# Kernel tuning notes

Hardware: AMD Instinct MI355X
Metric: run time of the kernel (lower is better)

The kernel has to match this reference:

```python
import jax, jax.numpy as jnp
import numpy as np
from jax import lax

D_MODEL = 512
D_STATE = 64
D_CONV = 4
EXPAND = 2
HEADDIM = 64
D_INNER = EXPAND * D_MODEL          # 1024
NHEADS = D_INNER // HEADDIM         # 16
CONV_DIM = D_INNER + 2 * D_STATE    # 1152 (x, B, C go through depthwise conv)
D_PROJ = 2 * D_INNER + 2 * D_STATE + NHEADS  # 2192
EPS = 1e-5


def silu(x):
    return x * jax.nn.sigmoid(x)


def layernorm(x, w, b):
    mu = jnp.mean(x, axis=-1, keepdims=True)
    var = jnp.mean((x - mu) ** 2, axis=-1, keepdims=True)
    return (x - mu) * lax.rsqrt(var + EPS) * w + b


def mamba2(x, in_w, conv_w, conv_b, dt_bias, A_log, D_h, mnorm_w, out_w):
    """Faithful Mamba2 forward (sequential selective-scan form of SSD).
    x: [B, L, D_MODEL]"""
    Bsz, L, _ = x.shape
    zxbcdt = x @ in_w  # [B, L, D_PROJ]
    z = zxbcdt[..., :D_INNER]
    xBC = zxbcdt[..., D_INNER:D_INNER + CONV_DIM]
    dt = zxbcdt[..., -NHEADS:]

    # causal depthwise conv1d over sequence, then SiLU
    xBC_pad = jnp.pad(xBC, ((0, 0), (D_CONV - 1, 0), (0, 0)))
    xBC = lax.conv_general_dilated(
        xBC_pad, conv_w, window_strides=(1,), padding='VALID',
        dimension_numbers=('NWC', 'WIO', 'NWC'), feature_group_count=CONV_DIM)
    xBC = silu(xBC + conv_b)

    xh = xBC[..., :D_INNER].reshape(Bsz, L, NHEADS, HEADDIM)      # [B,L,H,P]
    Bc = xBC[..., D_INNER:D_INNER + D_STATE]                      # [B,L,N]
    Cc = xBC[..., D_INNER + D_STATE:]                             # [B,L,N]

    dt = jax.nn.softplus(dt + dt_bias)          # [B,L,H]
    dA = jnp.exp(dt * (-jnp.exp(A_log)))        # [B,L,H]
    dtx = dt[..., None] * xh                    # [B,L,H,P]

    def step(h, ins):
        dA_t, dtx_t, B_t, C_t = ins  # [B,H], [B,H,P], [B,N], [B,N]
        h = h * dA_t[:, :, None, None] + dtx_t[..., None] * B_t[:, None, None, :]
        y = jnp.einsum('bhpn,bn->bhp', h, C_t)
        return h, y

    h0 = jnp.zeros((Bsz, NHEADS, HEADDIM, D_STATE), x.dtype)
    xs = (jnp.moveaxis(dA, 1, 0), jnp.moveaxis(dtx, 1, 0),
          jnp.moveaxis(Bc, 1, 0), jnp.moveaxis(Cc, 1, 0))
    _, ys = lax.scan(step, h0, xs)              # [L,B,H,P]
    y = jnp.moveaxis(ys, 0, 1) + D_h[None, None, :, None] * xh
    y = y.reshape(Bsz, L, D_INNER)

    # gated RMSNorm: rmsnorm(y * silu(z)) * weight
    g = y * silu(z)
    g = g * lax.rsqrt(jnp.mean(g * g, axis=-1, keepdims=True) + EPS) * mnorm_w
    return g @ out_w  # [B, L, D_MODEL]


def setup_inputs() -> dict:
    key = jax.random.key(0)
    ks = jax.random.split(key, 16)
    B, L = 2, 4096
    s = 0.02
    inp = {
        'x': jax.random.normal(ks[0], (B, L, D_MODEL), jnp.float32),
        'norm_in_w': jnp.ones((D_MODEL,), jnp.float32),
        'norm_in_b': jnp.zeros((D_MODEL,), jnp.float32),
        'norm_out_w': jnp.ones((D_MODEL,), jnp.float32),
        'norm_out_b': jnp.zeros((D_MODEL,), jnp.float32),
        'in_w': jax.random.normal(ks[1], (D_MODEL, D_PROJ), jnp.float32) * s,
        'conv_w': jax.random.normal(ks[2], (D_CONV, 1, CONV_DIM), jnp.float32) * 0.1,
        'conv_b': jnp.zeros((CONV_DIM,), jnp.float32),
        'dt_bias': jnp.log(jnp.expm1(jax.random.uniform(ks[3], (NHEADS,), jnp.float32, 0.001, 0.1))),
        'A_log': jnp.log(jnp.arange(1, NHEADS + 1, dtype=jnp.float32)),
        'D_h': jnp.ones((NHEADS,), jnp.float32),
        'mnorm_w': jnp.ones((D_INNER,), jnp.float32),
        'out_w': jax.random.normal(ks[4], (D_INNER, D_MODEL), jnp.float32) * s,
        'ff_w1': jax.random.normal(ks[5], (D_MODEL, 4 * D_MODEL), jnp.float32) * s,
        'ff_b1': jnp.zeros((4 * D_MODEL,), jnp.float32),
        'ff_w2': jax.random.normal(ks[6], (4 * D_MODEL, D_MODEL), jnp.float32) * s,
        'ff_b2': jnp.zeros((D_MODEL,), jnp.float32),
    }
    return inp


def reference(x, norm_in_w, norm_in_b, norm_out_w, norm_out_b, in_w, conv_w,
              conv_b, dt_bias, A_log, D_h, mnorm_w, out_w, ff_w1, ff_b1,
              ff_w2, ff_b2):
    xn = layernorm(x, norm_in_w, norm_in_b)
    fwd = mamba2(xn, in_w, conv_w, conv_b, dt_bias, A_log, D_h, mnorm_w, out_w)
    bwd = mamba2(jnp.flip(xn, axis=1), in_w, conv_w, conv_b, dt_bias, A_log,
                 D_h, mnorm_w, out_w)
    m = layernorm(fwd + jnp.flip(bwd, axis=1), norm_out_w, norm_out_b)
    ff = jax.nn.gelu(m @ ff_w1 + ff_b1, approximate=False) @ ff_w2 + ff_b2
    return ff + x
```

## Files before the change

### kernel.cpp

```cpp
#include <hip/hip_runtime.h>
#include <hip/hip_bf16.h>

#define LSEQ 4096
#define BSZ 2
#define DMODEL 512
#define DINNER 1024
#define DSTATE 64
#define NHEADS 16
#define CONVDIM 1152
#define DPROJ 2192
#define NPAD 2304
#define NTOK (BSZ*LSEQ)
#define NCH 64

typedef __attribute__((ext_vector_type(8))) short short8;
typedef __attribute__((ext_vector_type(4))) float f32x4;

__device__ inline unsigned short f2b(float v){
  unsigned int u = __builtin_bit_cast(unsigned int, v);
  unsigned int r = (u + 0x7FFFu + ((u >> 16) & 1u)) >> 16;
  return (unsigned short)r;
}
__device__ inline float b2f(unsigned short u){
  unsigned int x = ((unsigned int)u) << 16;
  return __builtin_bit_cast(float, x);
}
__device__ inline uint4 pack8(const float* v){
  uint4 pk;
  pk.x = (unsigned)f2b(v[0]) | ((unsigned)f2b(v[1])<<16);
  pk.y = (unsigned)f2b(v[2]) | ((unsigned)f2b(v[3])<<16);
  pk.z = (unsigned)f2b(v[4]) | ((unsigned)f2b(v[5])<<16);
  pk.w = (unsigned)f2b(v[6]) | ((unsigned)f2b(v[7])<<16);
  return pk;
}
__device__ inline float gelu_f(float x){
  float x2 = x*x;
  float u = x*(0.7978845608f + 0.0356774081f*x2);
  float au = fabsf(u);
  float z = __expf(-2.f*au);
  float t = (1.f - z)/(1.f + z);
  t = (u >= 0.f) ? t : -t;
  return 0.5f*x*(1.f + t);
}

#define GLL16(gp, lp) __builtin_amdgcn_global_load_lds( \
    (const __attribute__((address_space(1))) unsigned int*)(gp), \
    (__attribute__((address_space(3))) unsigned int*)(lp), 16, 0, 0)

__global__ __launch_bounds__(256) void wconv_t(const float* __restrict__ src,
    unsigned short* __restrict__ dst, int K, int Nsrc, int Npad){
  __shared__ float t[32][33];
  int n0 = blockIdx.x*32, k0 = blockIdx.y*32;
  int tx = threadIdx.x & 31, ty = threadIdx.x >> 5;
  for (int i=0;i<4;i++){
    int k = k0 + ty + i*8; int n = n0 + tx;
    t[ty + i*8][tx] = (n < Nsrc) ? src[(size_t)k*Nsrc + n] : 0.f;
  }
  __syncthreads();
  for (int i=0;i<4;i++){
    int n = n0 + ty + i*8; int k = k0 + tx;
    if (n < Npad) dst[(size_t)n*K + k] = f2b(t[tx][ty + i*8]);
  }
}

__global__ __launch_bounds__(256) void layernorm_k(const float* __restrict__ in,
    const float* __restrict__ w, const float* __restrict__ bb, unsigned short* __restrict__ out){
  int row = blockIdx.x; int tid = threadIdx.x;
  const float* r = in + (size_t)row*DMODEL;
  float v0 = r[tid], v1 = r[tid+256];
  float s = v0+v1, sq = v0*v0+v1*v1;
  for (int m=32;m>=1;m>>=1){ s += __shfl_xor(s,m); sq += __shfl_xor(sq,m); }
  __shared__ float ws_[4], wq_[4];
  int wave = tid>>6, lane = tid&63;
  if (lane==0){ ws_[wave]=s; wq_[wave]=sq; }
  __syncthreads();
  s = ws_[0]+ws_[1]+ws_[2]+ws_[3]; sq = wq_[0]+wq_[1]+wq_[2]+wq_[3];
  float mu = s * (1.f/DMODEL);
  float var = sq * (1.f/DMODEL) - mu*mu;
  float rs = rsqrtf(var + 1e-5f);
  out[(size_t)row*DMODEL + tid]     = f2b((v0-mu)*rs*w[tid] + bb[tid]);
  out[(size_t)row*DMODEL + tid+256] = f2b((v1-mu)*rs*w[tid+256] + bb[tid+256]);
}

__global__ __launch_bounds__(256) void layernorm2_k(const float* __restrict__ in0,
    const float* __restrict__ in1,
    const float* __restrict__ w, const float* __restrict__ bb, unsigned short* __restrict__ out){
  int row = blockIdx.x; int tid = threadIdx.x;
  const float* r0 = in0 + (size_t)row*DMODEL;
  const float* r1 = in1 + (size_t)row*DMODEL;
  float v0 = r0[tid] + r1[tid], v1 = r0[tid+256] + r1[tid+256];
  float s = v0+v1, sq = v0*v0+v1*v1;
  for (int m=32;m>=1;m>>=1){ s += __shfl_xor(s,m); sq += __shfl_xor(sq,m); }
  __shared__ float ws_[4], wq_[4];
  int wave = tid>>6, lane = tid&63;
  if (lane==0){ ws_[wave]=s; wq_[wave]=sq; }
  __syncthreads();
  s = ws_[0]+ws_[1]+ws_[2]+ws_[3]; sq = wq_[0]+wq_[1]+wq_[2]+wq_[3];
  float mu = s * (1.f/DMODEL);
  float var = sq * (1.f/DMODEL) - mu*mu;
  float rs = rsqrtf(var + 1e-5f);
  out[(size_t)row*DMODEL + tid]     = f2b((v0-mu)*rs*w[tid] + bb[tid]);
  out[(size_t)row*DMODEL + tid+256] = f2b((v1-mu)*rs*w[tid+256] + bb[tid+256]);
}

__global__ __launch_bounds__(256) void reduce4_k(const float* __restrict__ pa,
    const float* __restrict__ pb, const float* __restrict__ bias,
    const float* __restrict__ resid, float* __restrict__ out){
  const size_t MN4 = (size_t)NTOK*DMODEL/4;
  for (size_t i = (size_t)blockIdx.x*256 + threadIdx.x; i < MN4; i += (size_t)gridDim.x*256){
    float4 a0 = ((const float4*)pa)[i];
    float4 a1 = ((const float4*)pa)[i + MN4];
    float4 b0 = ((const float4*)pb)[i];
    float4 b1 = ((const float4*)pb)[i + MN4];
    float4 rv = ((const float4*)resid)[i];
    int col = (int)((i*4) & (DMODEL-1));
    const float4 bs = *(const float4*)(bias + col);
    float4 o;
    o.x = a0.x + a1.x + b0.x + b1.x + bs.x + rv.x;
    o.y = a0.y + a1.y + b0.y + b1.y + bs.y + rv.y;
    o.z = a0.z + a1.z + b0.z + b1.z + bs.z + rv.z;
    o.w = a0.w + a1.w + b0.w + b1.w + bs.w + rv.w;
    ((float4*)out)[i] = o;
  }
}

__global__ __launch_bounds__(512, 2) void gemm256_k(const unsigned short* __restrict__ A,
    const unsigned short* __restrict__ Bt, void* __restrict__ outp, void* __restrict__ outp_hi,
    int M, int N, int K, int klen, int epi, const float* __restrict__ bias){
  __shared__ __align__(16) unsigned short As[32768];
  __shared__ __align__(16) unsigned short Bs[32768];
  const int tid = threadIdx.x;
  const int lane = tid & 63, wave = tid >> 6;
  const int wr = wave >> 2, wc = wave & 3;
  const int l15 = lane & 15, q = lane >> 4;
  int nbx = gridDim.x;
  int bid = blockIdx.y * nbx + blockIdx.x;
  int cpx = (nbx * gridDim.y) >> 3;
  int swz = (bid & 7) * cpx + (bid >> 3);
  int bn = swz % nbx, bm = swz / nbx;
  const int kstart = blockIdx.z * klen;
  const int NT = klen >> 6;
  const int j0 = tid, j1 = tid + 512;
  const int rr0 = j0 >> 2, rr1 = j1 >> 2;
  const int sc0 = (j0 & 3) ^ ((rr0 >> 1) & 3);
  const int sc1 = (j1 & 3) ^ ((rr1 >> 1) & 3);
  const unsigned short* a0 = A  + (size_t)(bm*256 + rr0)*K + kstart + sc0*8;
  const unsigned short* a1 = A  + (size_t)(bm*256 + rr1)*K + kstart + sc1*8;
  const unsigned short* b0 = Bt + (size_t)(bn*256 + rr0)*K + kstart + sc0*8;
  const unsigned short* b1 = Bt + (size_t)(bn*256 + rr1)*K + kstart + sc1*8;
  unsigned short* lA0 = As + j0*8;
  unsigned short* lA1 = As + j1*8;
  unsigned short* lB0 = Bs + j0*8;
  unsigned short* lB1 = Bs + j1*8;
#define STGA(t,kh) { const int go=(t)*64+(kh)*32, lo=((t)&1)*16384+(kh)*8192; \
  GLL16(a0+go, lA0+lo); GLL16(a1+go, lA1+lo); }
#define STGB(t,kh) { const int go=(t)*64+(kh)*32, lo=((t)&1)*16384+(kh)*8192; \
  GLL16(b0+go, lB0+lo); GLL16(b1+go, lB1+lo); }
  f32x4 acc[8][4];
  #pragma unroll
  for (int i=0;i<8;i++)
    #pragma unroll
    for (int j=0;j<4;j++) acc[i][j] = (f32x4){0.f,0.f,0.f,0.f};
  STGA(0,0); STGB(0,0); STGA(0,1); STGB(0,1);
  STGA(1,0); STGB(1,0);
  asm volatile("s_waitcnt vmcnt(4)" ::: "memory");
  __builtin_amdgcn_s_barrier();
  const int cOfs = (q ^ ((l15 >> 1) & 3)) * 8;
  const int arow = wr*128 + l15;
  const int brow = wc*64  + l15;
  for (int t = 0; t < NT; ++t){
    const unsigned short* Ab = As + (t & 1)*16384;
    const unsigned short* Bb = Bs + (t & 1)*16384;
    short8 af[4], bf4[4];
    #pragma unroll
    for (int mi=0;mi<4;mi++) af[mi]  = *(const short8*)(Ab + (arow + mi*16)*32 + cOfs);
    #pragma unroll
    for (int nt=0;nt<4;nt++) bf4[nt] = *(const short8*)(Bb + (brow + nt*16)*32 + cOfs);
    if (t+1 < NT) STGA(t+1,1);
    __builtin_amdgcn_s_barrier();
    asm volatile("s_waitcnt lgkmcnt(0)" ::: "memory");
    __builtin_amdgcn_sched_barrier(0);
    __builtin_amdgcn_s_setprio(1);
    #pragma unroll
    for (int mi=0;mi<4;mi++)
      #pragma unroll
      for (int nt=0;nt<4;nt++)
        acc[mi][nt] = __builtin_amdgcn_mfma_f32_16x16x32_bf16(af[mi], bf4[nt], acc[mi][nt], 0,0,0);
    __builtin_amdgcn_s_setprio(0);
    __builtin_amdgcn_s_barrier();
    #pragma unroll
    for (int mi=0;mi<4;mi++) af[mi] = *(const short8*)(Ab + (arow + (4+mi)*16)*32 + cOfs);
    if (t+1 < NT) STGB(t+1,1);
    __builtin_amdgcn_s_barrier();
    asm volatile("s_waitcnt lgkmcnt(0)" ::: "memory");
    __builtin_amdgcn_sched_barrier(0);
    __builtin_amdgcn_s_setprio(1);
    #pragma unroll
    for (int mi=0;mi<4;mi++)
      #pragma unroll
      for (int nt=0;nt<4;nt++)
        acc[4+mi][nt] = __builtin_amdgcn_mfma_f32_16x16x32_bf16(af[mi], bf4[nt], acc[4+mi][nt], 0,0,0);
    __builtin_amdgcn_s_setprio(0);
    __builtin_amdgcn_s_barrier();
    #pragma unroll
    for (int mi=0;mi<4;mi++) af[mi]  = *(const short8*)(Ab + 8192 + (arow + mi*16)*32 + cOfs);
    #pragma unroll
    for (int nt=0;nt<4;nt++) bf4[nt] = *(const short8*)(Bb + 8192 + (brow + nt*16)*32 + cOfs);
    if (t+2 < NT) STGA(t+2,0);
    __builtin_amdgcn_s_barrier();
    asm volatile("s_waitcnt lgkmcnt(0)" ::: "memory");
    __builtin_amdgcn_sched_barrier(0);
    __builtin_amdgcn_s_setprio(1);
    #pragma unroll
    for (int mi=0;mi<4;mi++)
      #pragma unroll
      for (int nt=0;nt<4;nt++)
        acc[mi][nt] = __builtin_amdgcn_mfma_f32_16x16x32_bf16(af[mi], bf4[nt], acc[mi][nt], 0,0,0);
    __builtin_amdgcn_s_setprio(0);
    __builtin_amdgcn_s_barrier();
    #pragma unroll
    for (int mi=0;mi<4;mi++) af[mi] = *(const short8*)(Ab + 8192 + (arow + (4+mi)*16)*32 + cOfs);
    if (t+2 < NT) STGB(t+2,0);
    __builtin_amdgcn_s_barrier();
    asm volatile("s_waitcnt lgkmcnt(0)" ::: "memory");
    __builtin_amdgcn_sched_barrier(0);
    __builtin_amdgcn_s_setprio(1);
    #pragma unroll
    for (int mi=0;mi<4;mi++)
      #pragma unroll
      for (int nt=0;nt<4;nt++)
        acc[4+mi][nt] = __builtin_amdgcn_mfma_f32_16x16x32_bf16(af[mi], bf4[nt], acc[4+mi][nt], 0,0,0);
    __builtin_amdgcn_s_setprio(0);
    if (t+2 < NT)      { asm volatile("s_waitcnt vmcnt(4)" ::: "memory"); }
    else if (t+1 < NT) { asm volatile("s_waitcnt vmcnt(0)" ::: "memory"); }
    __builtin_amdgcn_s_barrier();
  }
#undef STGA
#undef STGB
  float* cb = (float*)As + wave*1040;
  const int rbase = q*4;
  const int gr0t = bm*256 + wr*128;
  const int gc0 = bn*256 + wc*64;
  #pragma unroll
  for (int mt=0; mt<8; mt++){
    #pragma unroll
    for (int nt=0;nt<4;nt++)
      #pragma unroll
      for (int r=0;r<4;r++)
        cb[(rbase+r)*65 + nt*16 + l15] = acc[mt][nt][r];
    int gr0 = gr0t + mt*16;
    if (epi == 0){
      float* po = (float*)((blockIdx.z < 2) ? outp : outp_hi)
                + (size_t)(blockIdx.z & 1) * ((size_t)M * N);
      int r4 = lane >> 4, c0f = (lane & 15)*4;
      #pragma unroll
      for (int h=0; h<4; h++){
        int row = h*4 + r4;
        float4 v;
        v.x = cb[row*65 + c0f + 0];
        v.y = cb[row*65 + c0f + 1];
        v.z = cb[row*65 + c0f + 2];
        v.w = cb[row*65 + c0f + 3];
        *(float4*)(po + (size_t)(gr0+row)*N + gc0 + c0f) = v;
      }
    } else {
      int r8 = lane >> 3, c0 = (lane & 7)*8;
      #pragma unroll
      for (int h=0; h<2; h++){
        int row = h*8 + r8;
        float v[8];
        #pragma unroll
        for (int u=0;u<8;u++) v[u] = cb[row*65 + c0 + u];
        if (epi == 1){
          #pragma unroll
          for (int u=0;u<8;u++) v[u] = gelu_f(v[u] + bias[gc0 + c0 + u]);
        }
        *(uint4*)((unsigned short*)outp + (size_t)(gr0+row)*N + gc0 + c0) = pack8(v);
      }
    }
  }
}

__global__ __launch_bounds__(256) void dt_k(const unsigned short* __restrict__ zx,
    const float* __restrict__ dt_bias, const float* __restrict__ A_log,
    float* __restrict__ dAb, float* __restrict__ dtb){
  int b = blockIdx.y;
  int t = blockIdx.x*16 + (threadIdx.x>>4);
  int h = threadIdx.x & 15;
  float raw = b2f(zx[((size_t)b*LSEQ + t)*NPAD + (DINNER+CONVDIM) + h]) + dt_bias[h];
  float dt = (raw > 20.f) ? raw : log1pf(expf(raw));
  float dA = expf(-expf(A_log[h]) * dt);
  size_t f = ((size_t)b*LSEQ + t)*NHEADS + h;
  size_t r = ((size_t)(BSZ+b)*LSEQ + (LSEQ-1-t))*NHEADS + h;
  dAb[f] = dA; dtb[f] = dt;
  dAb[r] = dA; dtb[r] = dt;
}

__global__ __launch_bounds__(256) void conv_x_k(const unsigned short* __restrict__ zx,
    const float* __restrict__ conv_w, const float* __restrict__ conv_b,
    const float* __restrict__ dtb, unsigned short* __restrict__ dtxb,
    unsigned short* __restrict__ zcomp){
  int b = blockIdx.y;
  int t0blk = blockIdx.x * 32;
  int tid = threadIdx.x;
  int half = tid >> 7, cg = tid & 127;
  int c0 = cg * 8;
  int head = c0 >> 6;
  float wk[4][8], bias8[8];
  #pragma unroll
  for (int k=0;k<4;k++)
    #pragma unroll
    for (int j=0;j<8;j++) wk[k][j] = conv_w[k*CONVDIM + c0 + j];
  #pragma unroll
  for (int j=0;j<8;j++) bias8[j] = conv_b[c0 + j];
  __shared__ float sdtf[32][16], sdtb[32][16];
  for (int r = tid; r < 512; r += 256){
    int i = r >> 4, h = r & 15;
    sdtf[i][h] = dtb[((size_t)b*LSEQ + t0blk + i)*NHEADS + h];
    sdtb[i][h] = dtb[((size_t)(BSZ+b)*LSEQ + (LSEQ-1-(t0blk+i)))*NHEADS + h];
  }
  __syncthreads();
  int t0 = t0blk + half*16;
  float w0[8],w1[8],w2[8],w3[8];
  #pragma unroll
  for (int j=0;j<8;j++){ w1[j]=0.f; w2[j]=0.f; w3[j]=0.f; }
  for (int it=0; it<22; ++it){
    int t = t0 - 3 + it;
    #pragma unroll
    for (int j=0;j<8;j++){ w0[j]=w1[j]; w1[j]=w2[j]; w2[j]=w3[j]; }
    if (t >= 0 && t < LSEQ){
      uint4 xv = *(const uint4*)(zx + ((size_t)b*LSEQ + t)*NPAD + DINNER + c0);
      const unsigned short* xs = (const unsigned short*)&xv;
      #pragma unroll
      for (int j=0;j<8;j++) w3[j] = b2f(xs[j]);
      if (t >= t0 && t < t0+16){
        uint4 zv = *(const uint4*)(zx + ((size_t)b*LSEQ + t)*NPAD + c0);
        *(uint4*)(zcomp + ((size_t)b*LSEQ + t)*DINNER + c0) = zv;
      }
    } else {
      #pragma unroll
      for (int j=0;j<8;j++) w3[j] = 0.f;
    }
    if (t >= t0 && t < t0+16){
      float dtf = sdtf[t - t0blk][head];
      float v[8];
      #pragma unroll
      for (int j=0;j<8;j++){
        float a = bias8[j] + wk[0][j]*w0[j] + wk[1][j]*w1[j] + wk[2][j]*w2[j] + wk[3][j]*w3[j];
        v[j] = (a / (1.f + expf(-a))) * dtf;
      }
      *(uint4*)(dtxb + ((size_t)b*LSEQ + t)*DINNER + c0) = pack8(v);
    }
    int tau = t - 3;
    if (tau >= t0 && tau < t0+16){
      float dtv = sdtb[tau - t0blk][head];
      float v[8];
      #pragma unroll
      for (int j=0;j<8;j++){
        float a = bias8[j] + wk[0][j]*w3[j] + wk[1][j]*w2[j] + wk[2][j]*w1[j] + wk[3][j]*w0[j];
        v[j] = (a / (1.f + expf(-a))) * dtv;
      }
      *(uint4*)(dtxb + ((size_t)(BSZ+b)*LSEQ + (LSEQ-1-tau))*DINNER + c0) = pack8(v);
    }
  }
}

__global__ __launch_bounds__(256) void conv_bc_k(const unsigned short* __restrict__ zx,
    const float* __restrict__ conv_w, const float* __restrict__ conv_b,
    unsigned short* __restrict__ Bb, unsigned short* __restrict__ Cb){
  int b = blockIdx.y;
  int t0blk = blockIdx.x * 64;
  int tid = threadIdx.x;
  int slot = tid >> 4, cg = tid & 15;
  int c0 = cg*8;
  int ccol = DINNER + 1024 + c0;
  int cw = 1024 + c0;
  float wk[4][8], bias8[8];
  #pragma unroll
  for (int k=0;k<4;k++)
    #pragma unroll
    for (int j=0;j<8;j++) wk[k][j] = conv_w[k*CONVDIM + cw + j];
  #pragma unroll
  for (int j=0;j<8;j++) bias8[j] = conv_b[cw + j];
  int t0 = t0blk + slot*4;
  float w0[8],w1[8],w2[8],w3[8];
  #pragma unroll
  for (int j=0;j<8;j++){ w1[j]=0.f; w2[j]=0.f; w3[j]=0.f; }
  for (int it=0; it<10; ++it){
    int t = t0 - 3 + it;
    #pragma unroll
    for (int j=0;j<8;j++){ w0[j]=w1[j]; w1[j]=w2[j]; w2[j]=w3[j]; }
    if (t >= 0 && t < LSEQ){
      uint4 xv = *(const uint4*)(zx + ((size_t)b*LSEQ + t)*NPAD + ccol);
      const unsigned short* xs = (const unsigned short*)&xv;
      #pragma unroll
      for (int j=0;j<8;j++) w3[j] = b2f(xs[j]);
    } else {
      #pragma unroll
      for (int j=0;j<8;j++) w3[j] = 0.f;
    }
    if (t >= t0 && t < t0+4){
      float v[8];
      #pragma unroll
      for (int j=0;j<8;j++){
        float a = bias8[j] + wk[0][j]*w0[j] + wk[1][j]*w1[j] + wk[2][j]*w2[j] + wk[3][j]*w3[j];
        v[j] = a / (1.f + expf(-a));
      }
      size_t tok = (size_t)b*LSEQ + t;
      if (c0 < 64) *(uint4*)(Bb + tok*DSTATE + c0)      = pack8(v);
      else         *(uint4*)(Cb + tok*DSTATE + (c0-64)) = pack8(v);
    }
    int tau = t - 3;
    if (tau >= t0 && tau < t0+4){
      float v[8];
      #pragma unroll
      for (int j=0;j<8;j++){
        float a = bias8[j] + wk[0][j]*w3[j] + wk[1][j]*w2[j] + wk[2][j]*w1[j] + wk[3][j]*w0[j];
        v[j] = a / (1.f + expf(-a));
      }
      size_t tok = (size_t)(BSZ+b)*LSEQ + (LSEQ-1-tau);
      if (c0 < 64) *(uint4*)(Bb + tok*DSTATE + c0)      = pack8(v);
      else         *(uint4*)(Cb + tok*DSTATE + (c0-64)) = pack8(v);
    }
  }
}

__device__ inline void gemm64(const unsigned short* Ab, const unsigned short* Bb_,
                              int l15, int q, f32x4 acc[4][4]){
  #pragma unroll
  for (int ks=0; ks<2; ks++){
    short8 af[4], bf4[4];
    #pragma unroll
    for (int mt=0;mt<4;mt++) af[mt]  = *(const short8*)(Ab  + (mt*16+l15)*72 + ks*32 + q*8);
    #pragma unroll
    for (int nt=0;nt<4;nt++) bf4[nt] = *(const short8*)(Bb_ + (nt*16+l15)*72 + ks*32 + q*8);
    #pragma unroll
    for (int mt=0;mt<4;mt++)
      #pragma unroll
      for (int nt=0;nt<4;nt++)
        acc[mt][nt] = __builtin_amdgcn_mfma_f32_16x16x32_bf16(af[mt], bf4[nt], acc[mt][nt], 0,0,0);
  }
}

__global__ __launch_bounds__(64) void ssd1_k(const float* __restrict__ dAb,
    const unsigned short* __restrict__ dtxb, const unsigned short* __restrict__ Bb,
    const unsigned short* __restrict__ Cb,
    unsigned short* __restrict__ y0, unsigned short* __restrict__ y1,
    unsigned short* __restrict__ hbuf, float* __restrict__ Pch, float* __restrict__ ebuf){
  int ch = blockIdx.x, h = blockIdx.y, z = blockIdx.z;
  int d = z >> 1, b = z & 1;
  int lane = threadIdx.x;
  int l15 = lane & 15, q = lane >> 4;
  int tr = lane >> 3, cb8 = (lane & 7)*8;
  size_t tokb = (size_t)z*LSEQ + (size_t)ch*64;
  size_t zhc = ((size_t)z*NHEADS + h)*NCH + ch;
  __shared__ __align__(16) unsigned short S1[64*72];
  __shared__ __align__(16) unsigned short S2[64*72];
  __shared__ __align__(16) unsigned short S3[64*72];
  __shared__ float Lb[64];
  float L = fmaxf(logf(dAb[(tokb + lane)*NHEADS + h]), -60.f);
  #pragma unroll
  for (int off=1; off<64; off<<=1){
    float v = __shfl_up(L, off);
    if (lane >= off) L += v;
  }
  Lb[lane] = L;
  float e = expf(L);
  ebuf[zhc*64 + lane] = e;
  if (lane == 63) Pch[zhc] = e;
  for (int i=0;i<8;i++){
    int t = i*8 + tr;
    *(uint4*)&S1[t*72 + cb8] = *(const uint4*)(Cb + (tokb+t)*DSTATE + cb8);
    *(uint4*)&S2[t*72 + cb8] = *(const uint4*)(Bb + (tokb+t)*DSTATE + cb8);
    uint4 xv = *(const uint4*)(dtxb + (tokb+t)*DINNER + (size_t)h*64 + cb8);
    const unsigned short* xs = (const unsigned short*)&xv;
    #pragma unroll
    for (int j=0;j<8;j++) S3[(cb8+j)*72 + t] = xs[j];
  }
  f32x4 sa[4][4];
  for (int i=0;i<4;i++) for (int j=0;j<4;j++) sa[i][j] = (f32x4){0.f,0.f,0.f,0.f};
  gemm64(S1, S2, l15, q, sa);
  float Lsv[4];
  #pragma unroll
  for (int nt=0;nt<4;nt++) Lsv[nt] = Lb[nt*16 + l15];
  #pragma unroll
  for (int mt=0;mt<4;mt++){
    #pragma unroll
    for (int r=0;r<4;r++){
      int t = mt*16 + q*4 + r;
      float Lt = Lb[t];
      #pragma unroll
      for (int nt=0;nt<4;nt++){
        int s = nt*16 + l15;
        float v = (t >= s) ? expf(Lt - Lsv[nt]) * sa[mt][nt][r] : 0.f;
        S1[t*72 + s] = f2b(v);
      }
    }
  }
  f32x4 ya[4][4];
  for (int i=0;i<4;i++) for (int j=0;j<4;j++) ya[i][j] = (f32x4){0.f,0.f,0.f,0.f};
  gemm64(S1, S3, l15, q, ya);
  #pragma unroll
  for (int mt=0;mt<4;mt++)
    #pragma unroll
    for (int pt=0;pt<4;pt++)
      #pragma unroll
      for (int r=0;r<4;r++)
        S2[(mt*16+q*4+r)*72 + pt*16 + l15] = f2b(ya[mt][pt][r]);
  unsigned short* yb = d ? y1 : y0;
  for (int i=0;i<8;i++){
    int t = i*8 + tr; int g = ch*64 + t;
    int tph = d ? (LSEQ-1-g) : g;
    *(uint4*)(yb + ((size_t)b*LSEQ + tph)*DINNER + (size_t)h*64 + cb8) = *(uint4*)&S2[t*72 + cb8];
  }
  float L63 = Lb[63];
  for (int i=0;i<8;i++){
    int s = i*8 + tr;
    float w = expf(L63 - Lb[s]);
    uint4 bv = *(const uint4*)(Bb + (tokb+s)*DSTATE + cb8);
    const unsigned short* bs = (const unsigned short*)&bv;
    #pragma unroll
    for (int j=0;j<8;j++) S2[(cb8+j)*72 + s] = f2b(w * b2f(bs[j]));
  }
  f32x4 ga[4][4];
  for (int i=0;i<4;i++) for (int j=0;j<4;j++) ga[i][j] = (f32x4){0.f,0.f,0.f,0.f};
  gemm64(S3, S2, l15, q, ga);
  #pragma unroll
  for (int pt=0;pt<4;pt++)
    #pragma unroll
    for (int nt=0;nt<4;nt++)
      #pragma unroll
      for (int r=0;r<4;r++)
        S1[(pt*16+q*4+r)*72 + nt*16 + l15] = f2b(ga[pt][nt][r]);
  for (int i=0;i<8;i++){
    int p = i*8 + tr;
    *(uint4*)(hbuf + zhc*4096 + (size_t)p*64 + cb8) = *(uint4*)&S1[p*72 + cb8];
  }
}

__global__ __launch_bounds__(256) void comb_k(unsigned short* __restrict__ hbuf,
    const float* __restrict__ Pch){
  int u = blockIdx.x; int tid = threadIdx.x;
  int kb = blockIdx.y * 4;
  float hreg[4];
  #pragma unroll
  for (int k=0;k<4;k++) hreg[k]=0.f;
  for (int ch=0; ch<NCH; ch++){
    size_t base = ((size_t)u*NCH + ch)*4096;
    float P = Pch[(size_t)u*NCH + ch];
    #pragma unroll
    for (int k=0;k<4;k++){
      size_t idx = base + tid + (size_t)(kb+k)*256;
      float t = b2f(hbuf[idx]);
      hbuf[idx] = f2b(hreg[k]);
      hreg[k] = hreg[k]*P + t;
    }
  }
}

__global__ __launch_bounds__(64) void ssd2_k(const unsigned short* __restrict__ Cb,
    const unsigned short* __restrict__ hbuf, const unsigned short* __restrict__ dtxb,
    const float* __restrict__ dtb, const float* __restrict__ ebuf, const float* __restrict__ Dh,
    unsigned short* __restrict__ y0, unsigned short* __restrict__ y1){
  int ch = blockIdx.x, h = blockIdx.y, z = blockIdx.z;
  int d = z >> 1, b = z & 1;
  int lane = threadIdx.x;
  int l15 = lane & 15, q = lane >> 4;
  int tr = lane >> 3, cb8 = (lane & 7)*8;
  size_t tokb = (size_t)z*LSEQ + (size_t)ch*64;
  size_t zhc = ((size_t)z*NHEADS + h)*NCH + ch;
  __shared__ __align__(16) unsigned short S1[64*72];
  __shared__ __align__(16) unsigned short S2[64*72];
  __shared__ __align__(16) unsigned short S3[64*72];
  __shared__ float eb2[64], dti[64];
  eb2[lane] = ebuf[zhc*64 + lane];
  dti[lane] = 1.f / dtb[(tokb + lane)*NHEADS + h];
  float Dv = Dh[h];
  for (int i=0;i<8;i++){
    int t = i*8 + tr;
    *(uint4*)&S1[t*72 + cb8] = *(const uint4*)(Cb + (tokb+t)*DSTATE + cb8);
    *(uint4*)&S2[t*72 + cb8] = *(const uint4*)(hbuf + zhc*4096 + (size_t)t*64 + cb8);
  }
  f32x4 acc[4][4];
  for (int i=0;i<4;i++) for (int j=0;j<4;j++) acc[i][j] = (f32x4){0.f,0.f,0.f,0.f};
  gemm64(S1, S2, l15, q, acc);
  unsigned short* yb = d ? y1 : y0;
  #pragma unroll
  for (int mt=0;mt<4;mt++){
    #pragma unroll
    for (int r=0;r<4;r++){
      int t = mt*16 + q*4 + r; int g = ch*64 + t;
      int tph = d ? (LSEQ-1-g) : g;
      size_t rowb = ((size_t)b*LSEQ + tph)*DINNER + (size_t)h*64;
      size_t dxb_ = (tokb + t)*DINNER + (size_t)h*64;
      float et = eb2[t], di = dti[t];
      #pragma unroll
      for (int pt=0;pt<4;pt++){
        int p = pt*16 + l15;
        float v = acc[mt][pt][r]*et + b2f(yb[rowb + p]) + Dv * b2f(dtxb[dxb_ + p]) * di;
        S3[t*72 + p] = f2b(v);
      }
    }
  }
  for (int i=0;i<8;i++){
    int t = i*8 + tr; int g = ch*64 + t;
    int tph = d ? (LSEQ-1-g) : g;
    *(uint4*)(yb + ((size_t)b*LSEQ + tph)*DINNER + (size_t)h*64 + cb8) = *(uint4*)&S3[t*72 + cb8];
  }
}

__global__ __launch_bounds__(256) void gate_k(const unsigned short* __restrict__ y0,
    const unsigned short* __restrict__ y1, const unsigned short* __restrict__ zcomp,
    const float* __restrict__ mnw, unsigned short* __restrict__ gsum){
  int tok = blockIdx.x; int tid = threadIdx.x;
  __shared__ float g0s[DINNER], g1s[DINNER];
  float ss0 = 0.f, ss1 = 0.f;
  for (int i=0;i<4;i++){
    int c = tid + i*256;
    float z = b2f(zcomp[(size_t)tok*DINNER + c]);
    float sz = z / (1.f + expf(-z));
    float g0 = b2f(y0[(size_t)tok*DINNER + c]) * sz;
    float g1 = b2f(y1[(size_t)tok*DINNER + c]) * sz;
    g0s[c] = g0; g1s[c] = g1;
    ss0 += g0*g0; ss1 += g1*g1;
  }
  for (int m=32;m>=1;m>>=1){ ss0 += __shfl_xor(ss0,m); ss1 += __shfl_xor(ss1,m); }
  __shared__ float w0[4], w1[4];
  int wave = tid>>6, lane = tid&63;
  if (lane==0){ w0[wave]=ss0; w1[wave]=ss1; }
  __syncthreads();
  ss0 = w0[0]+w0[1]+w0[2]+w0[3];
  ss1 = w1[0]+w1[1]+w1[2]+w1[3];
  float r0 = rsqrtf(ss0*(1.f/DINNER) + 1e-5f);
  float r1 = rsqrtf(ss1*(1.f/DINNER) + 1e-5f);
  for (int i=0;i<4;i++){
    int c = tid + i*256;
    gsum[(size_t)tok*DINNER + c] = f2b((g0s[c]*r0 + g1s[c]*r1) * mnw[c]);
  }
}

extern "C" void kernel_launch(void* const* d_in, const int* in_sizes, int n_in,
                              void* d_out, int out_size, void* d_ws, size_t ws_size,
                              hipStream_t stream){
  const float* x       = (const float*)d_in[0];
  const float* nin_w   = (const float*)d_in[1];
  const float* nin_b   = (const float*)d_in[2];
  const float* nout_w  = (const float*)d_in[3];
  const float* nout_b  = (const float*)d_in[4];
  const float* in_w    = (const float*)d_in[5];
  const float* conv_w  = (const float*)d_in[6];
  const float* conv_b  = (const float*)d_in[7];
  const float* dt_bias = (const float*)d_in[8];
  const float* A_log   = (const float*)d_in[9];
  const float* D_h     = (const float*)d_in[10];
  const float* mnorm_w = (const float*)d_in[11];
  const float* out_w   = (const float*)d_in[12];
  const float* ff_w1   = (const float*)d_in[13];
  const float* ff_b1   = (const float*)d_in[14];
  const float* ff_w2   = (const float*)d_in[15];
  const float* ff_b2   = (const float*)d_in[16];
  float* out = (float*)d_out;

  char* ws = (char*)d_ws;
  size_t off = 0;
  auto alloc = [&](size_t bytes)->char*{
    char* p = ws + off; off = (off + bytes + 255) & ~(size_t)255; return p; };
  unsigned short* xn_bf = (unsigned short*)alloc((size_t)NTOK*DMODEL*2);
  unsigned short* in_wT = (unsigned short*)alloc((size_t)NPAD*DMODEL*2);
  unsigned short* out_wT= (unsigned short*)alloc((size_t)DMODEL*DINNER*2);
  unsigned short* w1T   = (unsigned short*)alloc((size_t)2048*DMODEL*2);
  unsigned short* w2T   = (unsigned short*)alloc((size_t)DMODEL*2048*2);
  unsigned short* zx    = (unsigned short*)alloc((size_t)NTOK*NPAD*2);
  unsigned short* zcomp = (unsigned short*)alloc((size_t)NTOK*DINNER*2);
  float*          dAb   = (float*)alloc((size_t)2*NTOK*NHEADS*4);
  float*          dtb   = (float*)alloc((size_t)2*NTOK*NHEADS*4);
  unsigned short* Bb    = (unsigned short*)alloc((size_t)2*NTOK*DSTATE*2);
  unsigned short* Cb    = (unsigned short*)alloc((size_t)2*NTOK*DSTATE*2);
  unsigned short* dtxb  = (unsigned short*)alloc((size_t)2*NTOK*DINNER*2);
  unsigned short* y0    = (unsigned short*)alloc((size_t)NTOK*DINNER*2);
  unsigned short* y1    = (unsigned short*)alloc((size_t)NTOK*DINNER*2);
  float*          Pch   = (float*)alloc((size_t)64*NCH*4);
  float*          ebuf  = (float*)alloc((size_t)64*NCH*64*4);
  size_t need = off;
  if (need > ws_size) return;

  unsigned short* hbuf  = zx;
  unsigned short* gsum  = dtxb;
  unsigned short* m_bf  = y0;
  unsigned short* h1    = zx;
  float* mp   = (float*)zx;
  float* fp01 = (float*)dtxb;
  float* fp23 = (float*)y0;

  wconv_t<<<dim3(NPAD/32,   DMODEL/32), 256, 0, stream>>>(in_w,  in_wT,  DMODEL, DPROJ,  NPAD);
  wconv_t<<<dim3(DMODEL/32, DINNER/32), 256, 0, stream>>>(out_w, out_wT, DINNER, DMODEL, DMODEL);
  wconv_t<<<dim3(2048/32,   DMODEL/32), 256, 0, stream>>>(ff_w1, w1T,    DMODEL, 2048,   2048);
  wconv_t<<<dim3(DMODEL/32, 2048/32),   256, 0, stream>>>(ff_w2, w2T,    2048,   DMODEL, DMODEL);
  layernorm_k<<<NTOK, 256, 0, stream>>>(x, nin_w, nin_b, xn_bf);
  gemm256_k<<<dim3(NPAD/256, NTOK/256, 1), 512, 0, stream>>>(xn_bf, in_wT, zx, nullptr, NTOK, NPAD, DMODEL, DMODEL, 3, nullptr);
  dt_k<<<dim3(LSEQ/16, BSZ), 256, 0, stream>>>(zx, dt_bias, A_log, dAb, dtb);
  conv_x_k<<<dim3(LSEQ/32, BSZ), 256, 0, stream>>>(zx, conv_w, conv_b, dtb, dtxb, zcomp);
  conv_bc_k<<<dim3(LSEQ/64, BSZ), 256, 0, stream>>>(zx, conv_w, conv_b, Bb, Cb);
  ssd1_k<<<dim3(NCH, NHEADS, 2*BSZ), 64, 0, stream>>>(dAb, dtxb, Bb, Cb, y0, y1, hbuf, Pch, ebuf);
  comb_k<<<dim3(64, 4), 256, 0, stream>>>(hbuf, Pch);
  ssd2_k<<<dim3(NCH, NHEADS, 2*BSZ), 64, 0, stream>>>(Cb, hbuf, dtxb, dtb, ebuf, D_h, y0, y1);
  gate_k<<<NTOK, 256, 0, stream>>>(y0, y1, zcomp, mnorm_w, gsum);
  gemm256_k<<<dim3(DMODEL/256, NTOK/256, 2), 512, 0, stream>>>(gsum, out_wT, mp, nullptr, NTOK, DMODEL, DINNER, 512, 0, nullptr);
  layernorm2_k<<<NTOK, 256, 0, stream>>>(mp, mp + (size_t)NTOK*DMODEL, nout_w, nout_b, m_bf);
  gemm256_k<<<dim3(2048/256, NTOK/256, 1), 512, 0, stream>>>(m_bf, w1T, h1, nullptr, NTOK, 2048, DMODEL, DMODEL, 1, ff_b1);
  gemm256_k<<<dim3(DMODEL/256, NTOK/256, 4), 512, 0, stream>>>(h1, w2T, fp01, fp23, NTOK, DMODEL, 2048, 512, 0, nullptr);
  reduce4_k<<<2048, 256, 0, stream>>>(fp01, fp23, ff_b2, x, out);
}
```

Baseline: 419.8 us.

## Swizzle SSD shared-memory tiles, prefetch chunk-combine loads, use fast exp

Transposed shared-memory tiles in the chunked SSD kernel now use an XOR swizzle on 8-element column groups, and the GEMM helper undoes the swizzle when reading. This is meant to reduce LDS bank conflicts on the transposed stores. The chunk-combine kernel software-prefetches the next chunk's state values and decay factor so the serial recurrence is not stalled on loads. expf is replaced by __expf in the conv, SSD and gate kernels, which trades some accuracy for fewer instructions.

```diff
diff --git a/kernel.cpp b/kernel.cpp
--- a/kernel.cpp
+++ b/kernel.cpp
@@ -347,7 +347,7 @@
       #pragma unroll
       for (int j=0;j<8;j++){
         float a = bias8[j] + wk[0][j]*w0[j] + wk[1][j]*w1[j] + wk[2][j]*w2[j] + wk[3][j]*w3[j];
-        v[j] = (a / (1.f + expf(-a))) * dtf;
+        v[j] = (a / (1.f + __expf(-a))) * dtf;
       }
       *(uint4*)(dtxb + ((size_t)b*LSEQ + t)*DINNER + c0) = pack8(v);
     }
@@ -358,7 +358,7 @@
       #pragma unroll
       for (int j=0;j<8;j++){
         float a = bias8[j] + wk[0][j]*w3[j] + wk[1][j]*w2[j] + wk[2][j]*w1[j] + wk[3][j]*w0[j];
-        v[j] = (a / (1.f + expf(-a))) * dtv;
+        v[j] = (a / (1.f + __expf(-a))) * dtv;
       }
       *(uint4*)(dtxb + ((size_t)(BSZ+b)*LSEQ + (LSEQ-1-tau))*DINNER + c0) = pack8(v);
     }
@@ -404,7 +404,7 @@
       #pragma unroll
       for (int j=0;j<8;j++){
         float a = bias8[j] + wk[0][j]*w0[j] + wk[1][j]*w1[j] + wk[2][j]*w2[j] + wk[3][j]*w3[j];
-        v[j] = a / (1.f + expf(-a));
+        v[j] = a / (1.f + __expf(-a));
       }
       size_t tok = (size_t)b*LSEQ + t;
       if (c0 < 64) *(uint4*)(Bb + tok*DSTATE + c0)      = pack8(v);
@@ -416,7 +416,7 @@
       #pragma unroll
       for (int j=0;j<8;j++){
         float a = bias8[j] + wk[0][j]*w3[j] + wk[1][j]*w2[j] + wk[2][j]*w1[j] + wk[3][j]*w0[j];
-        v[j] = a / (1.f + expf(-a));
+        v[j] = a / (1.f + __expf(-a));
       }
       size_t tok = (size_t)(BSZ+b)*LSEQ + (LSEQ-1-tau);
       if (c0 < 64) *(uint4*)(Bb + tok*DSTATE + c0)      = pack8(v);
@@ -425,21 +425,34 @@
   }
 }
 
+template<int SA, int SB>
+__device__ inline void gemm64s(const unsigned short* Ab, const unsigned short* Bb_,
+                               int l15, int q, f32x4 acc[4][4]){
+  #pragma unroll
+  for (int ks=0; ks<2; ks++){
+    short8 af[4], bf4[4];
+    #pragma unroll
+    for (int mt=0;mt<4;mt++){
+      int r = mt*16 + l15;
+      int c = ks*4 + q; if (SA) c ^= (r>>3)&7;
+      af[mt] = *(const short8*)(Ab + r*72 + c*8);
+    }
+    #pragma unroll
+    for (int nt=0;nt<4;nt++){
+      int r = nt*16 + l15;
+      int c = ks*4 + q; if (SB) c ^= (r>>3)&7;
+      bf4[nt] = *(const short8*)(Bb_ + r*72 + c*8);
+    }
+    #pragma unroll
+    for (int mt=0;mt<4;mt++)
+      #pragma unroll
+      for (int nt=0;nt<4;nt++)
+        acc[mt][nt] = __builtin_amdgcn_mfma_f32_16x16x32_bf16(af[mt], bf4[nt], acc[mt][nt], 0,0,0);
+  }
+}
 __device__ inline void gemm64(const unsigned short* Ab, const unsigned short* Bb_,
                               int l15, int q, f32x4 acc[4][4]){
-  #pragma unroll
-  for (int ks=0; ks<2; ks++){
-    short8 af[4], bf4[4];
-    #pragma unroll
-    for (int mt=0;mt<4;mt++) af[mt]  = *(const short8*)(Ab  + (mt*16+l15)*72 + ks*32 + q*8);
-    #pragma unroll
-    for (int nt=0;nt<4;nt++) bf4[nt] = *(const short8*)(Bb_ + (nt*16+l15)*72 + ks*32 + q*8);
-    #pragma unroll
-    for (int mt=0;mt<4;mt++)
-      #pragma unroll
-      for (int nt=0;nt<4;nt++)
-        acc[mt][nt] = __builtin_amdgcn_mfma_f32_16x16x32_bf16(af[mt], bf4[nt], acc[mt][nt], 0,0,0);
-  }
+  gemm64s<0,0>(Ab, Bb_, l15, q, acc);
 }
 
 __global__ __launch_bounds__(64) void ssd1_k(const float* __restrict__ dAb,
@@ -452,6 +465,7 @@
   int lane = threadIdx.x;
   int l15 = lane & 15, q = lane >> 4;
   int tr = lane >> 3, cb8 = (lane & 7)*8;
+  int m7 = lane & 7;
   size_t tokb = (size_t)z*LSEQ + (size_t)ch*64;
   size_t zhc = ((size_t)z*NHEADS + h)*NCH + ch;
   __shared__ __align__(16) unsigned short S1[64*72];
@@ -465,7 +479,7 @@
     if (lane >= off) L += v;
   }
   Lb[lane] = L;
-  float e = expf(L);
+  float e = __expf(L);
   ebuf[zhc*64 + lane] = e;
   if (lane == 63) Pch[zhc] = e;
   for (int i=0;i<8;i++){
@@ -474,32 +488,35 @@
     *(uint4*)&S2[t*72 + cb8] = *(const uint4*)(Bb + (tokb+t)*DSTATE + cb8);
     uint4 xv = *(const uint4*)(dtxb + (tokb+t)*DINNER + (size_t)h*64 + cb8);
     const unsigned short* xs = (const unsigned short*)&xv;
-    #pragma unroll
-    for (int j=0;j<8;j++) S3[(cb8+j)*72 + t] = xs[j];
+    int csw = ((i ^ m7) << 3) + tr;
+    #pragma unroll
+    for (int j=0;j<8;j++) S3[(cb8+j)*72 + csw] = xs[j];
   }
   f32x4 sa[4][4];
   for (int i=0;i<4;i++) for (int j=0;j<4;j++) sa[i][j] = (f32x4){0.f,0.f,0.f,0.f};
-  gemm64(S1, S2, l15, q, sa);
+  gemm64s<0,0>(S1, S2, l15, q, sa);
   float Lsv[4];
   #pragma unroll
   for (int nt=0;nt<4;nt++) Lsv[nt] = Lb[nt*16 + l15];
+  int sch = l15 >> 3, sin = l15 & 7;
   #pragma unroll
   for (int mt=0;mt<4;mt++){
     #pragma unroll
     for (int r=0;r<4;r++){
       int t = mt*16 + q*4 + r;
+      int trow = (t>>3)&7;
       float Lt = Lb[t];
       #pragma unroll
       for (int nt=0;nt<4;nt++){
         int s = nt*16 + l15;
-        float v = (t >= s) ? expf(Lt - Lsv[nt]) * sa[mt][nt][r] : 0.f;
-        S1[t*72 + s] = f2b(v);
+        float v = (t >= s) ? __expf(Lt - Lsv[nt]) * sa[mt][nt][r] : 0.f;
+        S1[t*72 + (((nt*2 + sch) ^ trow)<<3) + sin] = f2b(v);
       }
     }
   }
   f32x4 ya[4][4];
   for (int i=0;i<4;i++) for (int j=0;j<4;j++) ya[i][j] = (f32x4){0.f,0.f,0.f,0.f};
-  gemm64(S1, S3, l15, q, ya);
+  gemm64s<1,1>(S1, S3, l15, q, ya);
   #pragma unroll
   for (int mt=0;mt<4;mt++)
     #pragma unroll
@@ -516,15 +533,16 @@
   float L63 = Lb[63];
   for (int i=0;i<8;i++){
     int s = i*8 + tr;
-    float w = expf(L63 - Lb[s]);
+    float w = __expf(L63 - Lb[s]);
     uint4 bv = *(const uint4*)(Bb + (tokb+s)*DSTATE + cb8);
     const unsigned short* bs = (const unsigned short*)&bv;
-    #pragma unroll
-    for (int j=0;j<8;j++) S2[(cb8+j)*72 + s] = f2b(w * b2f(bs[j]));
+    int csw = ((i ^ m7) << 3) + tr;
+    #pragma unroll
+    for (int j=0;j<8;j++) S2[(cb8+j)*72 + csw] = f2b(w * b2f(bs[j]));
   }
   f32x4 ga[4][4];
   for (int i=0;i<4;i++) for (int j=0;j<4;j++) ga[i][j] = (f32x4){0.f,0.f,0.f,0.f};
-  gemm64(S3, S2, l15, q, ga);
+  gemm64s<1,1>(S3, S2, l15, q, ga);
   #pragma unroll
   for (int pt=0;pt<4;pt++)
     #pragma unroll
@@ -542,19 +560,28 @@
     const float* __restrict__ Pch){
   int u = blockIdx.x; int tid = threadIdx.x;
   int kb = blockIdx.y * 4;
+  size_t base0 = ((size_t)u*NCH)*4096;
   float hreg[4];
-  #pragma unroll
-  for (int k=0;k<4;k++) hreg[k]=0.f;
+  unsigned short ccur[4], cnxt[4] = {0,0,0,0};
+  #pragma unroll
+  for (int k=0;k<4;k++){ hreg[k]=0.f; ccur[k] = hbuf[base0 + tid + (size_t)(kb+k)*256]; }
+  float Pc = Pch[(size_t)u*NCH], Pn = 0.f;
   for (int ch=0; ch<NCH; ch++){
-    size_t base = ((size_t)u*NCH + ch)*4096;
-    float P = Pch[(size_t)u*NCH + ch];
+    size_t base = base0 + (size_t)ch*4096;
+    if (ch+1 < NCH){
+      size_t bnx = base + 4096;
+      #pragma unroll
+      for (int k=0;k<4;k++) cnxt[k] = hbuf[bnx + tid + (size_t)(kb+k)*256];
+      Pn = Pch[(size_t)u*NCH + ch + 1];
+    }
     #pragma unroll
     for (int k=0;k<4;k++){
-      size_t idx = base + tid + (size_t)(kb+k)*256;
-      float t = b2f(hbuf[idx]);
-      hbuf[idx] = f2b(hreg[k]);
-      hreg[k] = hreg[k]*P + t;
-    }
+      hbuf[base + tid + (size_t)(kb+k)*256] = f2b(hreg[k]);
+      hreg[k] = hreg[k]*Pc + b2f(ccur[k]);
+    }
+    #pragma unroll
+    for (int k=0;k<4;k++) ccur[k] = cnxt[k];
+    Pc = Pn;
   }
 }
 
@@ -618,7 +645,7 @@
   for (int i=0;i<4;i++){
     int c = tid + i*256;
     float z = b2f(zcomp[(size_t)tok*DINNER + c]);
-    float sz = z / (1.f + expf(-z));
+    float sz = z / (1.f + __expf(-z));
     float g0 = b2f(y0[(size_t)tok*DINNER + c]) * sz;
     float g1 = b2f(y1[(size_t)tok*DINNER + c]) * sz;
     g0s[c] = g0; g1s[c] = g1;
```

After: 403.1 us. 4.0% less time.
